# Kernel optimization log

Hardware: AMD Instinct MI355X
Metric: run time of the kernel (lower is better)

Reference implementation:

```python
import jax, jax.numpy as jnp
import numpy as np

SR = 22050
HOP = 512
BINS_PER_OCTAVE = 24
N_OCTAVES = 7
N_BINS = BINS_PER_OCTAVE * N_OCTAVES  # 168
FMIN = 32.7  # center_bins with bins_per_semitone=1 leaves fmin unchanged


def _make_cqt_kernels():
    """Right-aligned (causal) complex CQT kernels, 24 bins/octave, 7 octaves.

    This is the explicit math the stateful SlidingCqt24 C++ routine computes
    incrementally: for each bin k with center freq f_k = fmin * 2^(k/24),
    a Hann-windowed complex exponential of length N_k = ceil(Q*sr/f_k),
    Q = 1/(2^(1/24)-1). Bins are ordered ascending in frequency, matching the
    per-octave np.flip layout of the original forward.
    """
    Q = 1.0 / (2.0 ** (1.0 / BINS_PER_OCTAVE) - 1.0)
    freqs = FMIN * 2.0 ** (np.arange(N_BINS) / BINS_PER_OCTAVE)
    lens = np.ceil(Q * SR / freqs).astype(np.int64)
    n_max = int(lens.max())  # 23014
    kr = np.zeros((N_BINS, n_max), dtype=np.float32)
    ki = np.zeros((N_BINS, n_max), dtype=np.float32)
    for k in range(N_BINS):  # small fixed loop over 168 bins (setup only)
        n = int(lens[k])
        t = np.arange(n)
        win = np.hanning(n)
        c = win * np.exp(2j * np.pi * freqs[k] * t / SR) / n
        kr[k, n_max - n:] = c.real.astype(np.float32)
        ki[k, n_max - n:] = c.imag.astype(np.float32)
    return kr, ki


def setup_inputs() -> dict:
    key = jax.random.key(0)
    audio = jax.random.normal(key, (4, 1, 352768), dtype=jnp.float32)
    kr, ki = _make_cqt_kernels()
    return {
        "audio_waveforms": audio,
        "kern_real": jnp.asarray(kr),
        "kern_imag": jnp.asarray(ki),
    }


def reference(audio_waveforms, kern_real, kern_imag):
    # audio: [B, C, S]; kernels: [K, Nmax]
    n_max = kern_real.shape[1]
    B, C, S = audio_waveforms.shape
    n_blocks = S // HOP  # 689
    # Causal sliding window: block i analyzes the n_max samples ending at
    # sample (i+1)*HOP (left zero-pad for early blocks), matching the
    # block-streaming behavior of the sliding CQT.
    pad = n_max - HOP
    x = jnp.pad(audio_waveforms, ((0, 0), (0, 0), (pad, 0)))
    # Strided frame gather: [n_blocks, Nmax] index table.
    idx = jnp.arange(n_blocks)[:, None] * HOP + jnp.arange(n_max)[None, :]
    frames = x[..., idx]  # [B, C, T, Nmax]
    re = jnp.einsum("bctn,kn->bctk", frames, kern_real)
    im = jnp.einsum("bctn,kn->bctk", frames, kern_imag)
    mag = jnp.sqrt(re * re + im * im)  # [B, C, n_blocks, n_bins]
    return mag
```

## Files before the change

### kernel.cpp

```cpp
#include <hip/hip_runtime.h>
#include <math.h>


namespace {
constexpr int kSR    = 22050;
constexpr int kHop   = 512;
constexpr int kBins  = 168;
constexpr int kT     = 689;
constexpr int kB     = 4;
constexpr int kS     = 352768;
constexpr float kKScale    = 4096.0f;
constexpr float kKScaleInv = 1.0f / 4096.0f;
constexpr int kG16 = 11;
constexpr int kFBB = 88;
constexpr int kAcc = kB * kT * kBins * 2;
constexpr int kTPadB   = 768;
constexpr int kBinPadB = 176;
constexpr int kAccB    = kB * kTPadB * kBinPadB * 2;
}

typedef _Float16 half8 __attribute__((ext_vector_type(8)));
typedef _Float16 half2v __attribute__((ext_vector_type(2)));
typedef float floatx4 __attribute__((ext_vector_type(4)));

struct Jobs {
  int k0[48];
  int lo[48];
  int hi[48];
  int n;
};

struct JobsC {
  int lo16[kG16];
  int cb16[kG16];
  int mlo[3];
  int sm[24];
  int slo[24];
  int shi[24];
  int sbeg[3];
  int scnt[3];
  int ns;
  int totch;
};

__device__ inline void atomAddF(float* p, float v) {
  __hip_atomic_fetch_add(p, v, __ATOMIC_RELAXED, __HIP_MEMORY_SCOPE_AGENT);
}

typedef __attribute__((address_space(3))) unsigned int lds_uint;
typedef __attribute__((address_space(1))) const unsigned int glb_uint;
__device__ __forceinline__ void dma16(const void* g, void* l) {
  __builtin_amdgcn_global_load_lds((glb_uint*)g, (lds_uint*)l, 16, 0, 0);
}

__global__ __launch_bounds__(256) void prep_fused(
    const float* __restrict__ x, const float* __restrict__ kr,
    const float* __restrict__ ki, _Float16* __restrict__ xp,
    _Float16* __restrict__ bp, float* __restrict__ accb,
    const int pad, const int xps, const int nmax,
    const int nbx, const int nbp, const JobsC jt) {
  int bid = blockIdx.x;
  const int tid = threadIdx.x;

  if (bid < nbx) {
    const int octx = xps >> 3;
    const int gid = bid * 256 + tid;
    if (gid >= kB * octx) return;
    const int b = gid / octx;
    const int i = (gid - b * octx) * 8;
    const float* xb = x + (size_t)b * kS - pad;
    half8 h;
    #pragma unroll
    for (int j = 0; j < 8; ++j) {
      const int e = i + j;
      h[j] = (e >= pad && e < pad + kS) ? (_Float16)xb[e] : (_Float16)0.f;
    }
    *(half8*)&xp[(size_t)b * xps + i] = h;
    return;
  }
  bid -= nbx;

  if (bid < nbp) {
    const int chunkid = bid * 4 + (tid >> 6);
    const int lane = tid & 63;
    if (chunkid >= jt.totch) return;
    int g = 0;
    #pragma unroll
    for (int j = 1; j < kG16; ++j)
      if (chunkid >= jt.cb16[j]) g = j;
    const int c = chunkid - jt.cb16[g];
    const int mm = lane & 15;
    const int q  = lane >> 4;
    const int bin  = g * 16 + mm;
    const int col0 = jt.lo16[g] + c * 32 + q * 8;
    const bool binok = (bin < kBins);
    const float* rowr = kr + (size_t)bin * nmax;
    const float* rowi = ki + (size_t)bin * nmax;
    half8 hre, him;
    #pragma unroll
    for (int j = 0; j < 8; ++j) {
      const int col = col0 + j;
      const bool ok = binok && (col < nmax);
      hre[j] = ok ? (_Float16)(rowr[col] * kKScale) : (_Float16)0.f;
      him[j] = ok ? (_Float16)(rowi[col] * kKScale) : (_Float16)0.f;
    }
    _Float16* dst = bp + (size_t)chunkid * 1024 + lane * 8;
    *(half8*)dst = hre;
    *(half8*)(dst + 512) = him;
    return;
  }
  bid -= nbp;

  const int idx = (bid * 256 + tid) * 4;
  if (idx < kAcc)
    *(floatx4*)&accb[idx] = (floatx4){0.f, 0.f, 0.f, 0.f};
}

template <bool PARTIAL>
__global__ __launch_bounds__(256) void cqt_mfma_t(
    const _Float16* __restrict__ bp, const _Float16* __restrict__ xp,
    float* __restrict__ accb, _Float16* __restrict__ part,
    const int xps, const JobsC jt) {
  __shared__ _Float16 lds[2][10240];

  const int sx = blockIdx.y;
  const int fb = blockIdx.x >> 2;
  const int b  = blockIdx.x & 3;
  const int tid  = threadIdx.x;
  const int wave = tid >> 6;
  const int lane = tid & 63;
  const int mm = lane & 15;
  const int q  = lane >> 4;
  const int mac = jt.sm[sx];
  const int g16 = mac * 4 + wave;
  const bool gvalid = (g16 < kG16);
  const int mlo = jt.mlo[mac];
  const int gs = gvalid ? ((jt.lo16[g16] - mlo) >> 5) : 0x7fffffff;
  const int slo = jt.slo[sx];
  const int shi = jt.shi[sx];
  const int fbase = fb * 32;

  const _Float16* xb = xp + (size_t)b * xps;
  int aoff;
  {
    const int tl = wave & 1;
    int row = fbase + tl * 16 + mm;
    if (row > kT - 1) row = kT - 1;
    aoff = row * kHop + q * 8 + ((wave >> 1) * 32);
  }
  const _Float16* bgrp =
      gvalid ? (bp + (size_t)(jt.cb16[g16] - gs) * 1024 + lane * 8) : bp;

  floatx4 accr[2], acci[2];
  #pragma unroll
  for (int tl = 0; tl < 2; ++tl) {
    accr[tl] = (floatx4){0.f, 0.f, 0.f, 0.f};
    acci[tl] = (floatx4){0.f, 0.f, 0.f, 0.f};
  }

  auto stageDMA = [&](int c, int buf) {
    _Float16* L = lds[buf];
    dma16(xb + mlo + c * 32 + aoff, L + wave * 512);
    if (gvalid && c >= gs) {
      const _Float16* bs = bgrp + (size_t)c * 1024;
      #pragma unroll
      for (int cc = 0; cc < 2; ++cc)
        #pragma unroll
        for (int ri = 0; ri < 2; ++ri)
          dma16(bs + cc * 1024 + ri * 512,
                L + 2048 + (wave * 4 + cc * 2 + ri) * 512);
    }
  };

  auto compute = [&](int c, int buf) {
    if (!gvalid || c < gs) return;
    const _Float16* L = lds[buf];
    #pragma unroll
    for (int cc = 0; cc < 2; ++cc) {
      const half8 Bre = *(const half8*)(L + 2048 + (wave * 4 + cc * 2) * 512 + lane * 8);
      const half8 Bim = *(const half8*)(L + 2048 + (wave * 4 + cc * 2 + 1) * 512 + lane * 8);
      #pragma unroll
      for (int tl = 0; tl < 2; ++tl) {
        const half8 A = *(const half8*)(L + (cc * 2 + tl) * 512 + lane * 8);
        accr[tl] = __builtin_amdgcn_mfma_f32_16x16x32_f16(A, Bre, accr[tl], 0, 0, 0);
        acci[tl] = __builtin_amdgcn_mfma_f32_16x16x32_f16(A, Bim, acci[tl], 0, 0, 0);
      }
    }
  };

  stageDMA(slo, 0);
  int buf = 0;
  #pragma unroll 1
  for (int c = slo; c < shi; c += 2) {
    __syncthreads();
    if (c + 2 < shi) stageDMA(c + 2, buf ^ 1);
    compute(c, buf);
    buf ^= 1;
  }

  if (PARTIAL) {
    _Float16* pw = part +
        (((size_t)sx * kFBB + blockIdx.x) * 4 + wave) * 1024 + lane * 16;
    half8 p0, p1;
    #pragma unroll
    for (int r = 0; r < 4; ++r) {
      p0[r * 2]     = (_Float16)accr[0][r];
      p0[r * 2 + 1] = (_Float16)acci[0][r];
      p1[r * 2]     = (_Float16)accr[1][r];
      p1[r * 2 + 1] = (_Float16)acci[1][r];
    }
    *(half8*)pw = p0;
    *(half8*)(pw + 8) = p1;
  } else {
    const int bin = g16 * 16 + mm;
    if (bin < kBins) {
      #pragma unroll
      for (int tl = 0; tl < 2; ++tl) {
        const int tb = fbase + tl * 16 + q * 4;
        #pragma unroll
        for (int r = 0; r < 4; ++r) {
          const int t = tb + r;
          if (t < kT) {
            const size_t o = (((size_t)b * kT + t) * kBins + bin) * 2;
            atomAddF(&accb[o],     accr[tl][r] * kKScaleInv);
            atomAddF(&accb[o + 1], acci[tl][r] * kKScaleInv);
          }
        }
      }
    }
  }
}

__global__ __launch_bounds__(256) void cqt_mag_part(
    const _Float16* __restrict__ part, float* __restrict__ out,
    const JobsC jt) {
  const int fbb = blockIdx.x;
  const int fb = fbb >> 2;
  const int b  = fbb & 3;
  const int wave = threadIdx.x >> 6;
  const int lane = threadIdx.x & 63;
  const int g16 = blockIdx.y * 4 + wave;
  if (g16 >= kG16) return;
  const int mac = g16 >> 2;
  const int w   = g16 & 3;
  const int mm = lane & 15;
  const int q  = lane >> 4;

  float a[16];
  #pragma unroll
  for (int i = 0; i < 16; ++i) a[i] = 0.f;
  const int s0 = jt.sbeg[mac];
  const int s1 = s0 + jt.scnt[mac];
  #pragma unroll 1
  for (int s = s0; s < s1; ++s) {
    const _Float16* p = part +
        (((size_t)s * kFBB + fbb) * 4 + w) * 1024 + lane * 16;
    const half8 v0 = *(const half8*)p;
    const half8 v1 = *(const half8*)(p + 8);
    #pragma unroll
    for (int j = 0; j < 8; ++j) {
      a[j]     += (float)v0[j];
      a[8 + j] += (float)v1[j];
    }
  }
  const int k = g16 * 16 + mm;
  if (k >= kBins) return;
  #pragma unroll
  for (int tl = 0; tl < 2; ++tl) {
    #pragma unroll
    for (int r = 0; r < 4; ++r) {
      const int t = fb * 32 + tl * 16 + q * 4 + r;
      if (t < kT) {
        const float re = a[tl * 8 + r * 2];
        const float im = a[tl * 8 + r * 2 + 1];
        out[((size_t)b * kT + t) * kBins + k] =
            sqrtf(re * re + im * im) * kKScaleInv;
      }
    }
  }
}

__global__ __launch_bounds__(256) void cqt_mag4(
    const float* __restrict__ accb, float* __restrict__ out) {
  const int gid = (blockIdx.x * 256 + threadIdx.x) * 4;
  if (gid >= kB * kT * kBins) return;
  const floatx4 v0 = *(const floatx4*)&accb[gid * 2];
  const floatx4 v1 = *(const floatx4*)&accb[gid * 2 + 4];
  floatx4 o;
  o[0] = sqrtf(v0[0] * v0[0] + v0[1] * v0[1]);
  o[1] = sqrtf(v0[2] * v0[2] + v0[3] * v0[3]);
  o[2] = sqrtf(v1[0] * v1[0] + v1[1] * v1[1]);
  o[3] = sqrtf(v1[2] * v1[2] + v1[3] * v1[3]);
  *(floatx4*)&out[gid] = o;
}

__global__ __launch_bounds__(256) void cqt_mag_final(
    const float* __restrict__ accb, float* __restrict__ out,
    const int tp, const int kp) {
  int gid = blockIdx.x * 256 + threadIdx.x;
  if (gid >= kB * kT * kBins) return;
  const int k = gid % kBins;
  const int r = gid / kBins;
  const int t = r % kT;
  const int b = r / kT;
  const float2 v = ((const float2*)accb)[((size_t)b * tp + t) * kp + k];
  out[gid] = sqrtf(v.x * v.x + v.y * v.y);
}

__global__ __launch_bounds__(256) void prep_x_kernel(
    const float* __restrict__ x, _Float16* __restrict__ xp,
    const int pad, const int xps) {
  const int halfx = xps >> 1;
  int gid = blockIdx.x * 256 + threadIdx.x;
  if (gid >= kB * halfx) return;
  const int b = gid / halfx;
  const int i = (gid - b * halfx) * 2;
  float v0 = 0.f, v1 = 0.f;
  if (i     >= pad && i     < pad + kS) v0 = x[(size_t)b * kS + (i - pad)];
  if (i + 1 >= pad && i + 1 < pad + kS) v1 = x[(size_t)b * kS + (i + 1 - pad)];
  half2v h; h.x = (_Float16)v0; h.y = (_Float16)v1;
  *(half2v*)&xp[(size_t)b * xps + i] = h;
}

__global__ __launch_bounds__(256) void cqt_mfma_kernel(
    const float* __restrict__ kr, const float* __restrict__ ki,
    const _Float16* __restrict__ xp, float* __restrict__ accb,
    const int nmax, const int xps, const Jobs jt) {
  __shared__ _Float16 Bs[2][16][264];
  const int jb = blockIdx.x;
  const int k0   = jt.k0[jb];
  const int n_lo = jt.lo[jb];
  const int n_hi = jt.hi[jb];
  const int b  = blockIdx.z;
  const int fb = blockIdx.y;
  const int tid  = threadIdx.x;
  const int lane = tid & 63;
  const int wave = tid >> 6;
  const int m = lane & 15;
  const int q = lane >> 4;
  const int sbin = tid >> 4;
  const int scol = tid & 15;
  const int gbin = k0 + sbin;
  const bool binok = (gbin < kBins);
  const float* rowr = kr + (size_t)gbin * nmax;
  const float* rowi = ki + (size_t)gbin * nmax;
  const int fbase = fb * 256 + wave * 64;
  const _Float16* ax =
      xp + (size_t)b * xps + (size_t)(fbase + m) * kHop + q * 8;
  floatx4 accr[4], acci[4];
  #pragma unroll
  for (int tl = 0; tl < 4; ++tl) {
    accr[tl] = (floatx4){0.f, 0.f, 0.f, 0.f};
    acci[tl] = (floatx4){0.f, 0.f, 0.f, 0.f};
  }
  for (int n0r = n_lo; n0r < n_hi; n0r += 256) {
    __syncthreads();
    #pragma unroll
    for (int c = 0; c < 16; ++c) {
      const int col = n0r + scol + c * 16;
      const bool ok = binok && (col < nmax);
      const float vr = ok ? rowr[col] : 0.f;
      const float vi = ok ? rowi[col] : 0.f;
      Bs[0][sbin][scol + c * 16] = (_Float16)(vr * kKScale);
      Bs[1][sbin][scol + c * 16] = (_Float16)(vi * kKScale);
    }
    __syncthreads();
    const _Float16* axr = ax + n0r;
    #pragma unroll
    for (int c = 0; c < 8; ++c) {
      const int ko = c * 32 + q * 8;
      const half8 br = *(const half8*)&Bs[0][m][ko];
      const half8 bi = *(const half8*)&Bs[1][m][ko];
      #pragma unroll
      for (int tl = 0; tl < 4; ++tl) {
        const half8 a = *(const half8*)(axr + tl * 16 * kHop + c * 32);
        accr[tl] = __builtin_amdgcn_mfma_f32_16x16x32_f16(a, br, accr[tl], 0, 0, 0);
        acci[tl] = __builtin_amdgcn_mfma_f32_16x16x32_f16(a, bi, acci[tl], 0, 0, 0);
      }
    }
  }
  #pragma unroll
  for (int tl = 0; tl < 4; ++tl) {
    #pragma unroll
    for (int rr = 0; rr < 4; ++rr) {
      const int t = fbase + tl * 16 + q * 4 + rr;
      const size_t o = (((size_t)b * kTPadB + t) * kBinPadB + (k0 + m)) * 2;
      atomAddF(&accb[o],     accr[tl][rr] * kKScaleInv);
      atomAddF(&accb[o + 1], acci[tl][rr] * kKScaleInv);
    }
  }
}

namespace fb32 {
constexpr int TT = 8;
constexpr int KG = 4;
constexpr int kTTiles  = (kT + TT - 1) / TT;
constexpr int kKGroups = kBins / KG;
constexpr int kWaves   = kB * kTTiles * kKGroups;
}

__global__ __launch_bounds__(256) void cqt_mag_kernel(
    const float* __restrict__ x,
    const float* __restrict__ kr,
    const float* __restrict__ ki,
    float* __restrict__ out,
    const int nmax, const int pad) {
  using namespace fb32;
  const int wave = (blockIdx.x << 2) + (threadIdx.x >> 6);
  const int lane = threadIdx.x & 63;
  if (wave >= kWaves) return;
  const int kg    = wave / (kB * kTTiles);
  const int rem   = wave - kg * (kB * kTTiles);
  const int b     = rem / kTTiles;
  const int ttile = rem - b * kTTiles;
  const int k0 = kg * KG;
  const int t0 = ttile * TT;
  const double Q  = 1.0 / (exp2(1.0 / 24.0) - 1.0);
  const double f0 = 32.7 * exp2((double)k0 / 24.0);
  int N = (int)ceil(Q * (double)kSR / f0) + 8;
  int full_start = nmax - N;
  if (full_start < 0) full_start = 0;
  int tbase[TT], lo[TT], t_last;
  { int t = t0 + TT - 1; if (t > kT - 1) t = kT - 1; t_last = t; }
  #pragma unroll
  for (int tt = 0; tt < TT; ++tt) {
    int t = t0 + tt; if (t > kT - 1) t = kT - 1;
    tbase[tt] = b * kS + t * kHop - pad;
    lo[tt]    = pad - t * kHop;
  }
  int head_start = pad - t_last * kHop;
  if (head_start < full_start) head_start = full_start;
  int safe = pad - t0 * kHop;
  if (safe < head_start) safe = head_start;
  int body_start = nmax - ((nmax - safe) & ~63);
  float accr[TT][KG], acci[TT][KG];
  #pragma unroll
  for (int tt = 0; tt < TT; ++tt)
    #pragma unroll
    for (int kk = 0; kk < KG; ++kk) { accr[tt][kk] = 0.f; acci[tt][kk] = 0.f; }
  for (int n = body_start - 64; n > head_start - 64; n -= 64) {
    const int nn = n + lane;
    const bool kok = (nn >= 0);
    float krv[KG], kiv[KG];
    #pragma unroll
    for (int kk = 0; kk < KG; ++kk) {
      krv[kk] = kok ? kr[(k0 + kk) * nmax + nn] : 0.f;
      kiv[kk] = kok ? ki[(k0 + kk) * nmax + nn] : 0.f;
    }
    float a[TT];
    #pragma unroll
    for (int tt = 0; tt < TT; ++tt)
      a[tt] = (nn >= lo[tt]) ? x[tbase[tt] + nn] : 0.f;
    #pragma unroll
    for (int tt = 0; tt < TT; ++tt)
      #pragma unroll
      for (int kk = 0; kk < KG; ++kk) {
        accr[tt][kk] = fmaf(a[tt], krv[kk], accr[tt][kk]);
        acci[tt][kk] = fmaf(a[tt], kiv[kk], acci[tt][kk]);
      }
  }
  for (int n = body_start; n < nmax; n += 64) {
    const int nn = n + lane;
    float krv[KG], kiv[KG];
    #pragma unroll
    for (int kk = 0; kk < KG; ++kk) {
      krv[kk] = kr[(k0 + kk) * nmax + nn];
      kiv[kk] = ki[(k0 + kk) * nmax + nn];
    }
    float a[TT];
    #pragma unroll
    for (int tt = 0; tt < TT; ++tt)
      a[tt] = x[tbase[tt] + nn];
    #pragma unroll
    for (int tt = 0; tt < TT; ++tt)
      #pragma unroll
      for (int kk = 0; kk < KG; ++kk) {
        accr[tt][kk] = fmaf(a[tt], krv[kk], accr[tt][kk]);
        acci[tt][kk] = fmaf(a[tt], kiv[kk], acci[tt][kk]);
      }
  }
  #pragma unroll
  for (int tt = 0; tt < TT; ++tt) {
    #pragma unroll
    for (int kk = 0; kk < KG; ++kk) {
      float r = accr[tt][kk];
      float i = acci[tt][kk];
      #pragma unroll
      for (int s = 32; s > 0; s >>= 1) {
        r += __shfl_xor(r, s, 64);
        i += __shfl_xor(i, s, 64);
      }
      if (lane == 0) {
        const int t = t0 + tt;
        if (t < kT)
          out[(b * kT + t) * kBins + (k0 + kk)] = sqrtf(r * r + i * i);
      }
    }
  }
}

extern "C" void kernel_launch(void* const* d_in, const int* in_sizes, int n_in,
                              void* d_out, int out_size, void* d_ws, size_t ws_size,
                              hipStream_t stream) {
  const float* x  = (const float*)d_in[0];
  const float* kr = (const float*)d_in[1];
  const float* ki = (const float*)d_in[2];
  float* out = (float*)d_out;

  const int nmax = in_sizes[1] / kBins;
  const int pad  = nmax - kHop;

  const int kcap = ((nmax + 255) / 256) * 256;
  const double Q = 1.0 / (exp2(1.0 / 24.0) - 1.0);

  JobsC jc;
  int tot = 0;
  for (int g = 0; g < kG16; ++g) {
    const double f0 = 32.7 * exp2((double)(16 * g) / 24.0);
    const int N = (int)ceil(Q * (double)kSR / f0) + 8;
    int lo = nmax - N;
    if (lo < 0) lo = 0;
    lo &= ~255;
    jc.lo16[g] = lo;
    jc.cb16[g] = tot;
    tot += (kcap - lo) / 32;
  }
  jc.totch = tot;
  int ns = 0;
  for (int m = 0; m < 3; ++m) {
    jc.mlo[m] = jc.lo16[4 * m];
    jc.sbeg[m] = ns;
    const int C = (kcap - jc.mlo[m]) / 32;
    const int nsl = (C + 95) / 96;
    const int len = ((C + nsl - 1) / nsl + 1) & ~1;
    for (int s = 0; s < nsl && ns < 24; ++s) {
      const int lo = s * len;
      if (lo >= C) break;
      int hi = lo + len;
      if (hi > C) hi = C;
      jc.sm[ns] = m; jc.slo[ns] = lo; jc.shi[ns] = hi;
      ++ns;
    }
    jc.scnt[m] = ns - jc.sbeg[m];
  }
  jc.ns = ns;

  const int xpsA = (kT - 1) * kHop + kcap + 256;
  const size_t xpA_bytes = (size_t)kB * xpsA * sizeof(_Float16);
  const size_t bpA_bytes = (size_t)tot * 2048;

  const size_t partP_off   = (xpA_bytes + 511) & ~(size_t)511;
  const size_t partP_bytes = (size_t)ns * kFBB * 4 * 1024 * sizeof(_Float16);
  const size_t bpP_off     = (partP_off + partP_bytes + 511) & ~(size_t)511;
  const size_t ws_P = bpP_off + bpA_bytes;

  const size_t accA_off  = (xpA_bytes + 511) & ~(size_t)511;
  const size_t accA_bytes = (size_t)kAcc * sizeof(float);
  const size_t bpA_off   = (accA_off + accA_bytes + 511) & ~(size_t)511;
  const size_t ws_A = bpA_off + bpA_bytes;

  const int xpsB = (kTPadB - 1) * kHop + kcap + 256;
  const size_t xpB_bytes = (size_t)kB * xpsB * sizeof(_Float16);
  const size_t accB_off  = (xpB_bytes + 511) & ~(size_t)511;
  const size_t accB_bytes = (size_t)kAccB * sizeof(float);
  const size_t ws_B = accB_off + accB_bytes;

  const int nbx = (kB * (xpsA / 8) + 255) / 256;
  const int nbp = (tot + 3) / 4;

  if (ws_size >= ws_P) {
    _Float16* xp   = (_Float16*)d_ws;
    _Float16* part = (_Float16*)((char*)d_ws + partP_off);
    _Float16* bp   = (_Float16*)((char*)d_ws + bpP_off);

    prep_fused<<<nbx + nbp, 256, 0, stream>>>(
        x, kr, ki, xp, bp, (float*)part , pad, xpsA, nmax,
        nbx, nbp, jc);
    {
      dim3 grid(kFBB, ns);
      cqt_mfma_t<true><<<grid, 256, 0, stream>>>(
          bp, xp, nullptr, part, xpsA, jc);
    }
    {
      dim3 grid(kFBB, 3);
      cqt_mag_part<<<grid, 256, 0, stream>>>(part, out, jc);
    }
    return;
  }

  if (ws_size >= ws_A) {
    _Float16* xp = (_Float16*)d_ws;
    float* accb  = (float*)((char*)d_ws + accA_off);
    _Float16* bp = (_Float16*)((char*)d_ws + bpA_off);

    const int nba = (kAcc / 4 + 255) / 256;
    prep_fused<<<nbx + nbp + nba, 256, 0, stream>>>(
        x, kr, ki, xp, bp, accb, pad, xpsA, nmax, nbx, nbp, jc);
    {
      dim3 grid(kFBB, ns);
      cqt_mfma_t<false><<<grid, 256, 0, stream>>>(
          bp, xp, accb, nullptr, xpsA, jc);
    }
    {
      const int total = kB * kT * kBins;
      cqt_mag4<<<(total / 4 + 255) / 256, 256, 0, stream>>>(accb, out);
    }
    return;
  }

  if (ws_size >= ws_B) {
    _Float16* xp = (_Float16*)d_ws;
    float* accb  = (float*)((char*)d_ws + accB_off);
    Jobs jt;
    int nj = 0;
    for (int g = 0; g < 11; ++g) {
      const int gk0 = 16 * g;
      const double f0 = 32.7 * exp2((double)gk0 / 24.0);
      const int N = (int)ceil(Q * (double)kSR / f0) + 8;
      int lo = nmax - N;
      if (lo < 0) lo = 0;
      lo = (lo / 2048) * 2048;
      for (int s = lo; s < kcap && nj < 48; s += 2048) {
        jt.k0[nj] = gk0;
        jt.lo[nj] = s;
        jt.hi[nj] = (s + 2048 < kcap) ? s + 2048 : kcap;
        ++nj;
      }
    }
    jt.n = nj;
    hipMemsetAsync(accb, 0, accB_bytes, stream);
    {
      const int total = kB * (xpsB / 2);
      prep_x_kernel<<<(total + 255) / 256, 256, 0, stream>>>(x, xp, pad, xpsB);
    }
    {
      dim3 grid(nj, kTPadB / 256, kB);
      cqt_mfma_kernel<<<grid, 256, 0, stream>>>(kr, ki, xp, accb, nmax, xpsB, jt);
    }
    {
      const int total = kB * kT * kBins;
      cqt_mag_final<<<(total + 255) / 256, 256, 0, stream>>>(
          accb, out, kTPadB, kBinPadB);
    }
    return;
  }

  {
    const int blocks = fb32::kWaves / 4;
    cqt_mag_kernel<<<blocks, 256, 0, stream>>>(x, kr, ki, out, nmax, pad);
  }
}
```

Before: 121.7 us.

## Add 128-frame-tile MFMA CQT path with finer K-slicing and fp16 partials

Adds a new primary path where each block computes a 128-frame tile (8 MFMA row tiles per wave) instead of the prior smaller tile, so each staged kernel chunk is reused across more frames and B loads are amortized. The reduction dimension is split into more, shorter slices (max 28 chunks, up to 40 slices) to keep enough blocks in flight, with fp16 partials reduced by a new magnitude kernel. In exchange it uses more accumulator registers per thread, writes a larger partial buffer, and needs more workspace; older paths remain as fallbacks.

```diff
diff --git a/kernel.cpp b/kernel.cpp
--- a/kernel.cpp
+++ b/kernel.cpp
@@ -13,7 +13,9 @@
 constexpr float kKScaleInv = 1.0f / 4096.0f;
 constexpr int kG16 = 11;
 constexpr int kFBB = 88;
+constexpr int kFBB2 = 24;
 constexpr int kAcc = kB * kT * kBins * 2;
+constexpr int kMaxSl = 40;
 constexpr int kTPadB   = 768;
 constexpr int kBinPadB = 176;
 constexpr int kAccB    = kB * kTPadB * kBinPadB * 2;
@@ -34,9 +36,9 @@
   int lo16[kG16];
   int cb16[kG16];
   int mlo[3];
-  int sm[24];
-  int slo[24];
-  int shi[24];
+  int sm[kMaxSl];
+  int slo[kMaxSl];
+  int shi[kMaxSl];
   int sbeg[3];
   int scnt[3];
   int ns;
@@ -114,6 +116,148 @@
   const int idx = (bid * 256 + tid) * 4;
   if (idx < kAcc)
     *(floatx4*)&accb[idx] = (floatx4){0.f, 0.f, 0.f, 0.f};
+}
+
+__global__ __launch_bounds__(256) void cqt_mfma128(
+    const _Float16* __restrict__ bp, const _Float16* __restrict__ xp,
+    _Float16* __restrict__ part, const int xps, const JobsC jt) {
+  __shared__ _Float16 lds[2][8192];
+
+  const int sx  = blockIdx.y;
+  const int fbb = blockIdx.x;
+  const int fb  = fbb >> 2;
+  const int b   = fbb & 3;
+  const int tid  = threadIdx.x;
+  const int wave = tid >> 6;
+  const int lane = tid & 63;
+  const int mm = lane & 15;
+  const int q  = lane >> 4;
+  const int mac = jt.sm[sx];
+  const int g16 = mac * 4 + wave;
+  const bool gvalid = (g16 < kG16);
+  const int mlo = jt.mlo[mac];
+  const int gs = gvalid ? ((jt.lo16[g16] - mlo) >> 5) : 0x7fffffff;
+  const int slo = jt.slo[sx];
+  const int shi = jt.shi[sx];
+  const int fbase = fb * 128;
+
+  const _Float16* xb = xp + (size_t)b * xps;
+  int aoff[2];
+  #pragma unroll
+  for (int j = 0; j < 2; ++j) {
+    const int tl = wave + j * 4;
+    int row = fbase + tl * 16 + mm;
+    if (row > kT - 1) row = kT - 1;
+    aoff[j] = row * kHop + q * 8;
+  }
+  const _Float16* bgrp =
+      gvalid ? (bp + (size_t)(jt.cb16[g16] - gs) * 1024 + lane * 8) : bp;
+
+  floatx4 accr[8], acci[8];
+  #pragma unroll
+  for (int tl = 0; tl < 8; ++tl) {
+    accr[tl] = (floatx4){0.f, 0.f, 0.f, 0.f};
+    acci[tl] = (floatx4){0.f, 0.f, 0.f, 0.f};
+  }
+
+  auto stageDMA = [&](int c, int buf) {
+    _Float16* L = lds[buf];
+    #pragma unroll
+    for (int j = 0; j < 2; ++j)
+      dma16(xb + mlo + c * 32 + aoff[j], L + (wave + j * 4) * 512);
+    if (gvalid && c >= gs) {
+      const _Float16* bs = bgrp + (size_t)c * 1024;
+      dma16(bs,       L + 4096 + wave * 1024);
+      dma16(bs + 512, L + 4096 + wave * 1024 + 512);
+    }
+  };
+
+  auto compute = [&](int c, int buf) {
+    if (!gvalid || c < gs) return;
+    const _Float16* L = lds[buf];
+    const half8 Bre = *(const half8*)(L + 4096 + wave * 1024 + lane * 8);
+    const half8 Bim = *(const half8*)(L + 4096 + wave * 1024 + 512 + lane * 8);
+    #pragma unroll
+    for (int tl = 0; tl < 8; ++tl) {
+      const half8 A = *(const half8*)(L + tl * 512 + lane * 8);
+      accr[tl] = __builtin_amdgcn_mfma_f32_16x16x32_f16(A, Bre, accr[tl], 0, 0, 0);
+      acci[tl] = __builtin_amdgcn_mfma_f32_16x16x32_f16(A, Bim, acci[tl], 0, 0, 0);
+    }
+  };
+
+  stageDMA(slo, 0);
+  int buf = 0;
+  #pragma unroll 1
+  for (int c = slo; c < shi; ++c) {
+    __syncthreads();
+    if (c + 1 < shi) stageDMA(c + 1, buf ^ 1);
+    compute(c, buf);
+    buf ^= 1;
+  }
+
+  _Float16* pw = part +
+      (((size_t)sx * kFBB2 + fbb) * 4 + wave) * 4096 + lane * 8;
+  #pragma unroll
+  for (int tl = 0; tl < 8; ++tl) {
+    half8 p;
+    #pragma unroll
+    for (int r = 0; r < 4; ++r) {
+      p[r * 2]     = (_Float16)accr[tl][r];
+      p[r * 2 + 1] = (_Float16)acci[tl][r];
+    }
+    *(half8*)(pw + tl * 512) = p;
+  }
+}
+
+__global__ __launch_bounds__(256) void cqt_mag_part128(
+    const _Float16* __restrict__ part, float* __restrict__ out,
+    const JobsC jt) {
+  const int fbb = blockIdx.x;
+  const int fb = fbb >> 2;
+  const int b  = fbb & 3;
+  const int wave = threadIdx.x >> 6;
+  const int lane = threadIdx.x & 63;
+  const int g16 = blockIdx.y * 4 + wave;
+  if (g16 >= kG16) return;
+  const int mac = g16 >> 2;
+  const int w   = g16 & 3;
+  const int mm = lane & 15;
+  const int q  = lane >> 4;
+
+  float a[8][8];
+  #pragma unroll
+  for (int tl = 0; tl < 8; ++tl)
+    #pragma unroll
+    for (int j = 0; j < 8; ++j) a[tl][j] = 0.f;
+
+  const int s0 = jt.sbeg[mac];
+  const int s1 = s0 + jt.scnt[mac];
+  #pragma unroll 1
+  for (int s = s0; s < s1; ++s) {
+    const _Float16* p = part +
+        (((size_t)s * kFBB2 + fbb) * 4 + w) * 4096 + lane * 8;
+    #pragma unroll
+    for (int tl = 0; tl < 8; ++tl) {
+      const half8 v = *(const half8*)(p + tl * 512);
+      #pragma unroll
+      for (int j = 0; j < 8; ++j) a[tl][j] += (float)v[j];
+    }
+  }
+  const int k = g16 * 16 + mm;
+  if (k >= kBins) return;
+  #pragma unroll
+  for (int tl = 0; tl < 8; ++tl) {
+    #pragma unroll
+    for (int r = 0; r < 4; ++r) {
+      const int t = fb * 128 + tl * 16 + q * 4 + r;
+      if (t < kT) {
+        const float re = a[tl][r * 2];
+        const float im = a[tl][r * 2 + 1];
+        out[((size_t)b * kT + t) * kBins + k] =
+            sqrtf(re * re + im * im) * kKScaleInv;
+      }
+    }
+  }
 }
 
 template <bool PARTIAL>
@@ -526,38 +670,50 @@
     tot += (kcap - lo) / 32;
   }
   jc.totch = tot;
-  int ns = 0;
-  for (int m = 0; m < 3; ++m) {
-    jc.mlo[m] = jc.lo16[4 * m];
-    jc.sbeg[m] = ns;
-    const int C = (kcap - jc.mlo[m]) / 32;
-    const int nsl = (C + 95) / 96;
-    const int len = ((C + nsl - 1) / nsl + 1) & ~1;
-    for (int s = 0; s < nsl && ns < 24; ++s) {
-      const int lo = s * len;
-      if (lo >= C) break;
-      int hi = lo + len;
-      if (hi > C) hi = C;
-      jc.sm[ns] = m; jc.slo[ns] = lo; jc.shi[ns] = hi;
-      ++ns;
-    }
-    jc.scnt[m] = ns - jc.sbeg[m];
-  }
-  jc.ns = ns;
+  for (int m = 0; m < 3; ++m) jc.mlo[m] = jc.lo16[4 * m];
+
+  auto build_slices = [&](JobsC& j, int maxlen, int al) {
+    int ns = 0;
+    for (int m = 0; m < 3; ++m) {
+      j.sbeg[m] = ns;
+      const int C = (kcap - j.mlo[m]) / 32;
+      const int nsl = (C + maxlen - 1) / maxlen;
+      const int len = (((C + nsl - 1) / nsl) + al - 1) & ~(al - 1);
+      for (int s = 0; s < nsl && ns < kMaxSl; ++s) {
+        const int lo = s * len;
+        if (lo >= C) break;
+        int hi = lo + len;
+        if (hi > C) hi = C;
+        j.sm[ns] = m; j.slo[ns] = lo; j.shi[ns] = hi;
+        ++ns;
+      }
+      j.scnt[m] = ns - j.sbeg[m];
+    }
+    j.ns = ns;
+  };
 
   const int xpsA = (kT - 1) * kHop + kcap + 256;
-  const size_t xpA_bytes = (size_t)kB * xpsA * sizeof(_Float16);
-  const size_t bpA_bytes = (size_t)tot * 2048;
-
-  const size_t partP_off   = (xpA_bytes + 511) & ~(size_t)511;
-  const size_t partP_bytes = (size_t)ns * kFBB * 4 * 1024 * sizeof(_Float16);
+  const size_t xp_bytes = (size_t)kB * xpsA * sizeof(_Float16);
+  const size_t bp_bytes = (size_t)tot * 2048;
+
+  JobsC jc2 = jc;
+  build_slices(jc2, 28, 1);
+  const size_t part2_off   = (xp_bytes + 511) & ~(size_t)511;
+  const size_t part2_bytes = (size_t)jc2.ns * kFBB2 * 4 * 4096 * sizeof(_Float16);
+  const size_t bp2_off     = (part2_off + part2_bytes + 511) & ~(size_t)511;
+  const size_t ws_P2 = bp2_off + bp_bytes;
+
+  JobsC jcP = jc;
+  build_slices(jcP, 96, 2);
+  const size_t partP_off   = (xp_bytes + 511) & ~(size_t)511;
+  const size_t partP_bytes = (size_t)jcP.ns * kFBB * 4 * 1024 * sizeof(_Float16);
   const size_t bpP_off     = (partP_off + partP_bytes + 511) & ~(size_t)511;
-  const size_t ws_P = bpP_off + bpA_bytes;
-
-  const size_t accA_off  = (xpA_bytes + 511) & ~(size_t)511;
+  const size_t ws_P = bpP_off + bp_bytes;
+
+  const size_t accA_off  = (xp_bytes + 511) & ~(size_t)511;
   const size_t accA_bytes = (size_t)kAcc * sizeof(float);
   const size_t bpA_off   = (accA_off + accA_bytes + 511) & ~(size_t)511;
-  const size_t ws_A = bpA_off + bpA_bytes;
+  const size_t ws_A = bpA_off + bp_bytes;
 
   const int xpsB = (kTPadB - 1) * kHop + kcap + 256;
   const size_t xpB_bytes = (size_t)kB * xpsB * sizeof(_Float16);
@@ -568,6 +724,25 @@
   const int nbx = (kB * (xpsA / 8) + 255) / 256;
   const int nbp = (tot + 3) / 4;
 
+  if (ws_size >= ws_P2) {
+    _Float16* xp   = (_Float16*)d_ws;
+    _Float16* part = (_Float16*)((char*)d_ws + part2_off);
+    _Float16* bp   = (_Float16*)((char*)d_ws + bp2_off);
+
+    prep_fused<<<nbx + nbp, 256, 0, stream>>>(
+        x, kr, ki, xp, bp, (float*)part , pad, xpsA, nmax,
+        nbx, nbp, jc2);
+    {
+      dim3 grid(kFBB2, jc2.ns);
+      cqt_mfma128<<<grid, 256, 0, stream>>>(bp, xp, part, xpsA, jc2);
+    }
+    {
+      dim3 grid(kFBB2, 3);
+      cqt_mag_part128<<<grid, 256, 0, stream>>>(part, out, jc2);
+    }
+    return;
+  }
+
   if (ws_size >= ws_P) {
     _Float16* xp   = (_Float16*)d_ws;
     _Float16* part = (_Float16*)((char*)d_ws + partP_off);
@@ -575,15 +750,15 @@
 
     prep_fused<<<nbx + nbp, 256, 0, stream>>>(
         x, kr, ki, xp, bp, (float*)part , pad, xpsA, nmax,
-        nbx, nbp, jc);
+        nbx, nbp, jcP);
     {
-      dim3 grid(kFBB, ns);
+      dim3 grid(kFBB, jcP.ns);
       cqt_mfma_t<true><<<grid, 256, 0, stream>>>(
-          bp, xp, nullptr, part, xpsA, jc);
+          bp, xp, nullptr, part, xpsA, jcP);
     }
     {
       dim3 grid(kFBB, 3);
-      cqt_mag_part<<<grid, 256, 0, stream>>>(part, out, jc);
+      cqt_mag_part<<<grid, 256, 0, stream>>>(part, out, jcP);
     }
     return;
   }
@@ -595,11 +770,11 @@
 
     const int nba = (kAcc / 4 + 255) / 256;
     prep_fused<<<nbx + nbp + nba, 256, 0, stream>>>(
-        x, kr, ki, xp, bp, accb, pad, xpsA, nmax, nbx, nbp, jc);
+        x, kr, ki, xp, bp, accb, pad, xpsA, nmax, nbx, nbp, jcP);
     {
-      dim3 grid(kFBB, ns);
+      dim3 grid(kFBB, jcP.ns);
       cqt_mfma_t<false><<<grid, 256, 0, stream>>>(
-          bp, xp, accb, nullptr, xpsA, jc);
+          bp, xp, accb, nullptr, xpsA, jcP);
     }
     {
       const int total = kB * kT * kBins;
```

Result: slower. 177.8 us (+46.1%).
